# Optimization experiments

Hardware: AMD Instinct MI355X
Metric: run time of the kernel (lower is better)

The kernel has to match this reference:

```python
import jax, jax.numpy as jnp
import numpy as np

TOP_K = 2
NUM_EXPERTS = 8
ROUTE_SCALE = 1.0


def setup_inputs() -> dict:
    key = jax.random.key(0)
    ks = jax.random.split(key, 8)
    bs, slen, dim, hidden, E = 4, 1024, 2048, 1024, NUM_EXPERTS
    s = 0.02
    return {
        "x": jax.random.normal(ks[0], (bs, slen, dim), jnp.float32),
        "gate_w": jax.random.normal(ks[1], (E, dim), jnp.float32) * s,
        "w1": jax.random.normal(ks[2], (E, hidden, dim), jnp.float32) * s,
        "w2": jax.random.normal(ks[3], (E, dim, hidden), jnp.float32) * s,
        "w3": jax.random.normal(ks[4], (E, hidden, dim), jnp.float32) * s,
        "ws1": jax.random.normal(ks[5], (hidden, dim), jnp.float32) * s,
        "ws2": jax.random.normal(ks[6], (dim, hidden), jnp.float32) * s,
        "ws3": jax.random.normal(ks[7], (hidden, dim), jnp.float32) * s,
    }


def reference(x, gate_w, w1, w2, w3, ws1, ws2, ws3):
    bs, slen, dim = x.shape
    xf = x.reshape(-1, dim)  # (T, dim)
    # --- router: sigmoid scores in fp32, top-k (expert_bias is zeros at init) ---
    logits = (xf @ gate_w.T).astype(jnp.float32)  # (T, E)
    scores = jax.nn.sigmoid(logits)
    top_scores, sel_idx = jax.lax.top_k(scores, TOP_K)  # (T, k), (T, k)
    top_scores = top_scores * ROUTE_SCALE  # route_norm=False
    # --- routed experts: score_before_experts=True -> scale input by score ---
    routed = jnp.zeros_like(xf)
    for k in range(TOP_K):
        xs = xf * top_scores[:, k][:, None]  # (T, dim)
        h1 = jnp.einsum('td,ehd->teh', xs, w1)
        h3 = jnp.einsum('td,ehd->teh', xs, w3)
        h = jax.nn.silu(h1) * h3  # (T, E, hidden)
        onehot = jax.nn.one_hot(sel_idx[:, k], NUM_EXPERTS, dtype=h.dtype)  # (T, E)
        routed = routed + jnp.einsum('teh,te,edh->td', h, onehot, w2)
    # --- shared expert (SwiGLU FFN) ---
    shared = (jax.nn.silu(xf @ ws1.T) * (xf @ ws3.T)) @ ws2.T
    out = (shared + routed).reshape(bs, slen, dim)
    return out
```

## Files before the change

kernel.cpp:

```cpp
#include <hip/hip_runtime.h>
#include <hip/hip_bf16.h>
#include <cstdint>

#define TTOK   4096
#define DIM    2048
#define HID    1024
#define NEXP   8
#define GROWS  12288

typedef __attribute__((ext_vector_type(8))) __bf16 bf16x8;
typedef __attribute__((ext_vector_type(4))) float  f32x4;

__device__ __forceinline__ void glds16(const void* g, void* l) {
  __builtin_amdgcn_global_load_lds((const __attribute__((address_space(1))) void*)g,
                                   (__attribute__((address_space(3))) void*)l,
                                   16, 0, 0);
}

#define BAR() do { asm volatile("" ::: "memory"); __builtin_amdgcn_s_barrier(); \
                   asm volatile("" ::: "memory"); } while (0)

__global__ void convert_router_k(const float* __restrict__ w1, const float* __restrict__ w2,
                                 const float* __restrict__ w3, const float* __restrict__ ws1,
                                 const float* __restrict__ ws2, const float* __restrict__ ws3,
                                 __bf16* __restrict__ w13, __bf16* __restrict__ w2c,
                                 const float* __restrict__ x, const float* __restrict__ gw,
                                 int* __restrict__ sel, float* __restrict__ sco,
                                 int* __restrict__ counts) {
  const int N1 = 9 * 2048 * 2048 / 8;
  const int N2 = 9 * 2048 * 1024 / 8;
  const int CONV_BLOCKS = (N1 + N2) / 256;

  if (blockIdx.x < (unsigned)CONV_BLOCKS) {
    int s = blockIdx.x * 256 + threadIdx.x;
    const float* src;
    __bf16* dst;
    if (s < N1) {
      int e  = s / 524288;
      int r  = (s % 524288) / 256;
      int c  = (s % 256) * 8;
      int nr;
      if (r < 1024) { src = (e < 8 ? w1 + ((size_t)e * 1024 + r) * 2048 : ws1 + (size_t)r * 2048) + c;
                      nr = 2 * r; }
      else          { src = (e < 8 ? w3 + ((size_t)e * 1024 + (r - 1024)) * 2048 : ws3 + (size_t)(r - 1024) * 2048) + c;
                      nr = 2 * (r - 1024) + 1; }
      dst = w13 + ((size_t)e * 2048 + nr) * 2048 + c;
    } else {
      int s2 = s - N1;
      int e  = s2 / 262144;
      int r  = (s2 % 262144) / 128;
      int c  = (s2 % 128) * 8;
      src = (e < 8 ? w2 + ((size_t)e * 2048 + r) * 1024 : ws2 + (size_t)r * 1024) + c;
      dst = w2c + ((size_t)e * 2048 + r) * 1024 + c;
    }
    float4 a = *(const float4*)(src);
    float4 b = *(const float4*)(src + 4);
    bf16x8 o;
    o[0]=(__bf16)a.x; o[1]=(__bf16)a.y; o[2]=(__bf16)a.z; o[3]=(__bf16)a.w;
    o[4]=(__bf16)b.x; o[5]=(__bf16)b.y; o[6]=(__bf16)b.z; o[7]=(__bf16)b.w;
    *(bf16x8*)dst = o;
    return;
  }

  int t    = (blockIdx.x - CONV_BLOCKS) * 4 + (threadIdx.x >> 6);
  int lane = threadIdx.x & 63;
  const float* xr = x + (size_t)t * DIM;
  float acc[NEXP];
  #pragma unroll
  for (int e = 0; e < NEXP; ++e) acc[e] = 0.f;
  for (int d = lane * 4; d < DIM; d += 256) {
    float4 xv = *(const float4*)(xr + d);
    #pragma unroll
    for (int e = 0; e < NEXP; ++e) {
      float4 gv = *(const float4*)(gw + (size_t)e * DIM + d);
      acc[e] += xv.x * gv.x + xv.y * gv.y + xv.z * gv.z + xv.w * gv.w;
    }
  }
  #pragma unroll
  for (int off = 32; off; off >>= 1)
    #pragma unroll
    for (int e = 0; e < NEXP; ++e) acc[e] += __shfl_xor(acc[e], off);
  if (lane == 0) {
    float s[NEXP];
    #pragma unroll
    for (int e = 0; e < NEXP; ++e) s[e] = 1.f / (1.f + expf(-acc[e]));
    int e0 = 0;
    #pragma unroll
    for (int e = 1; e < NEXP; ++e) if (s[e] > s[e0]) e0 = e;
    int e1 = (e0 == 0) ? 1 : 0;
    #pragma unroll
    for (int e = 0; e < NEXP; ++e) if (e != e0 && s[e] > s[e1]) e1 = e;
    sel[2 * t] = e0; sel[2 * t + 1] = e1;
    sco[2 * t] = s[e0]; sco[2 * t + 1] = s[e1];
    atomicAdd(&counts[e0], 1); atomicAdd(&counts[e1], 1);
  }
}

__global__ void scan_k(const int* __restrict__ counts, int* __restrict__ offs) {
  if (threadIdx.x == 0 && blockIdx.x == 0) {
    int o = 0;
    for (int e = 0; e < NEXP; ++e) { offs[e] = o; o += counts[e]; }
    offs[NEXP] = o;
    offs[NEXP + 1] = o + TTOK;
  }
}

__global__ void gather_k(const float* __restrict__ x, const int* __restrict__ sel,
                         const float* __restrict__ sco, const int* __restrict__ offs,
                         int* __restrict__ cursor, int* __restrict__ token_rows,
                         __bf16* __restrict__ xg) {
  __shared__ int   rows[3];
  __shared__ float ss[3];
  int t = blockIdx.x;
  if (threadIdx.x == 0) {
    int e0 = sel[2 * t], e1 = sel[2 * t + 1];
    int r0 = offs[e0] + atomicAdd(&cursor[e0], 1);
    int r1 = offs[e1] + atomicAdd(&cursor[e1], 1);
    int r2 = 8192 + t;
    rows[0] = r0; rows[1] = r1; rows[2] = r2;
    ss[0] = sco[2 * t]; ss[1] = sco[2 * t + 1]; ss[2] = 1.0f;
    token_rows[3 * t] = r0; token_rows[3 * t + 1] = r1; token_rows[3 * t + 2] = r2;
  }
  __syncthreads();
  int c = threadIdx.x * 8;
  float4 v0 = *(const float4*)(x + (size_t)t * DIM + c);
  float4 v1 = *(const float4*)(x + (size_t)t * DIM + c + 4);
  #pragma unroll
  for (int j = 0; j < 3; ++j) {
    float s = ss[j];
    bf16x8 o;
    o[0]=(__bf16)(v0.x*s); o[1]=(__bf16)(v0.y*s); o[2]=(__bf16)(v0.z*s); o[3]=(__bf16)(v0.w*s);
    o[4]=(__bf16)(v1.x*s); o[5]=(__bf16)(v1.y*s); o[6]=(__bf16)(v1.z*s); o[7]=(__bf16)(v1.w*s);
    *(bf16x8*)(xg + (size_t)rows[j] * DIM + c) = o;
  }
}

template <int EPI>
__launch_bounds__(256)
__global__ void gemm_nt(const __bf16* __restrict__ A, const __bf16* __restrict__ Bw,
                        __bf16* __restrict__ Hb, float* __restrict__ c2a, float* __restrict__ c2b,
                        const int* __restrict__ offs, int K_, int N_) {
  int z  = blockIdx.z;
  int o0 = offs[z];
  int ne = offs[z + 1] - o0;

  int flat = blockIdx.y * 32 + blockIdx.x;
  int nid  = (flat & 7) * 64 + (flat >> 3);
  int bm   = nid & 31;
  int bn   = nid >> 5;

  if (bm * 128 >= ne) return;

  const __bf16* Aseg = A  + (size_t)(o0 + bm * 128) * K_;
  const __bf16* Bseg = Bw + ((size_t)z * N_ + bn * 128) * K_;

  __shared__ __align__(16) __bf16 sA[2][128 * 64];
  __shared__ __align__(16) __bf16 sB[2][128 * 64];

  int tid  = threadIdx.x;
  int wave = tid >> 6, lane = tid & 63;
  int wm = wave & 1, wn = wave >> 1;
  int fr = lane & 15;
  int fq = lane >> 4;
  int sw = fr & 7;

  f32x4 acc[4][4];
  #pragma unroll
  for (int i = 0; i < 4; ++i)
    #pragma unroll
    for (int j = 0; j < 4; ++j) acc[i][j] = (f32x4){0.f, 0.f, 0.f, 0.f};

#define STAGE(buf, kbase)                                                     \
  {                                                                           \
    _Pragma("unroll")                                                         \
    for (int it = 0; it < 4; ++it) {                                          \
      int s   = it * 256 + tid;                                               \
      int row = s >> 3;                                                       \
      int c8  = (s & 7) ^ (row & 7);                                          \
      glds16(Aseg + (size_t)row * K_ + (kbase) + c8 * 8, &sA[buf][s * 8]);    \
      glds16(Bseg + (size_t)row * K_ + (kbase) + c8 * 8, &sB[buf][s * 8]);    \
    }                                                                         \
  }

  STAGE(0, 0)
  asm volatile("s_waitcnt vmcnt(0)" ::: "memory");
  BAR();

  const int nk = K_ >> 6;
  for (int t = 0; t < nk; ++t) {
    int cur = t & 1;
    if (t + 1 < nk) {
      STAGE(cur ^ 1, (t + 1) << 6)
      asm volatile("s_waitcnt vmcnt(8)" ::: "memory");
    } else {
      asm volatile("s_waitcnt vmcnt(0)" ::: "memory");
    }
    BAR();

    const __bf16* rAbase = &sA[cur][(wm * 64 + fr) * 64];
    const __bf16* rBbase = &sB[cur][(wn * 64 + fr) * 64];
    #pragma unroll
    for (int kk = 0; kk < 2; ++kk) {
      int slot = ((kk * 4 + fq) ^ sw) * 8;
      bf16x8 af[4], bb[4];
      #pragma unroll
      for (int i = 0; i < 4; ++i) af[i] = *(const bf16x8*)(rAbase + i * 16 * 64 + slot);
      #pragma unroll
      for (int i = 0; i < 4; ++i) bb[i] = *(const bf16x8*)(rBbase + i * 16 * 64 + slot);
      #pragma unroll
      for (int mi = 0; mi < 4; ++mi)
        #pragma unroll
        for (int ni = 0; ni < 4; ++ni)
          acc[mi][ni] = __builtin_amdgcn_mfma_f32_16x16x32_bf16(af[mi], bb[ni], acc[mi][ni], 0, 0, 0);
    }
    BAR();
  }
#undef STAGE

  #pragma unroll
  for (int mi = 0; mi < 4; ++mi) {
    #pragma unroll
    for (int r = 0; r < 4; ++r) {
      int rl = bm * 128 + wm * 64 + mi * 16 + fq * 4 + r;
      bool ok = rl < ne;
      int grow = o0 + rl;
      if (EPI == 0) {
        #pragma unroll
        for (int ni = 0; ni < 4; ++ni) {
          float v = acc[mi][ni][r];
          float o = __shfl_xor(v, 1);
          float h1 = (fr & 1) ? o : v;
          float h3 = (fr & 1) ? v : o;
          float g  = h1 / (1.f + expf(-h1)) * h3;
          if (ok && !(fr & 1)) {
            int hcol = bn * 64 + wn * 32 + ni * 8 + (fr >> 1);
            Hb[(size_t)grow * 1024 + hcol] = (__bf16)g;
          }
        }
      } else {
        if (ok) {
          float* dst = (grow < 8192) ? (c2a + (size_t)grow * 2048)
                                     : (c2b + (size_t)(grow - 8192) * 2048);
          #pragma unroll
          for (int ni = 0; ni < 4; ++ni) {
            int col = bn * 128 + wn * 64 + ni * 16 + fr;
            dst[col] = acc[mi][ni][r];
          }
        }
      }
    }
  }
}

__global__ void combine_k(const float* __restrict__ c2a, const float* __restrict__ c2b,
                          const int* __restrict__ token_rows, float* __restrict__ out) {
  __shared__ int rr[3];
  int t = blockIdx.x;
  if (threadIdx.x < 3) rr[threadIdx.x] = token_rows[3 * t + threadIdx.x];
  __syncthreads();
  int c = threadIdx.x * 8;
  const float* p0 = c2a + (size_t)rr[0] * 2048 + c;
  const float* p1 = c2a + (size_t)rr[1] * 2048 + c;
  const float* p2 = c2b + (size_t)(rr[2] - 8192) * 2048 + c;
  float4 a0 = *(const float4*)p0,       a1 = *(const float4*)p1,       a2 = *(const float4*)p2;
  float4 b0 = *(const float4*)(p0 + 4), b1 = *(const float4*)(p1 + 4), b2 = *(const float4*)(p2 + 4);
  float4 oa, ob;
  oa.x = a0.x + a1.x + a2.x; oa.y = a0.y + a1.y + a2.y;
  oa.z = a0.z + a1.z + a2.z; oa.w = a0.w + a1.w + a2.w;
  ob.x = b0.x + b1.x + b2.x; ob.y = b0.y + b1.y + b2.y;
  ob.z = b0.z + b1.z + b2.z; ob.w = b0.w + b1.w + b2.w;
  float* op = out + (size_t)t * 2048 + c;
  *(float4*)op = oa;
  *(float4*)(op + 4) = ob;
}

extern "C" void kernel_launch(void* const* d_in, const int* in_sizes, int n_in,
                              void* d_out, int out_size, void* d_ws, size_t ws_size,
                              hipStream_t stream) {
  const float* x   = (const float*)d_in[0];
  const float* gw  = (const float*)d_in[1];
  const float* w1  = (const float*)d_in[2];
  const float* w2  = (const float*)d_in[3];
  const float* w3  = (const float*)d_in[4];
  const float* ws1 = (const float*)d_in[5];
  const float* ws2 = (const float*)d_in[6];
  const float* ws3 = (const float*)d_in[7];
  float* out = (float*)d_out;

  char* p = (char*)d_ws;
  int*   counts     = (int*)p;
  int*   cursor     = (int*)(p + 64);
  int*   offs       = (int*)(p + 128);
  int*   sel        = (int*)(p + 1024);
  float* sco        = (float*)(p + 1024 + 32768);
  int*   token_rows = (int*)(p + 1024 + 65536);
  char* big = p + (1 << 20);
  __bf16* w13  = (__bf16*)big;
  __bf16* w2c  = (__bf16*)(big + 75497472ull);
  __bf16* xg   = (__bf16*)(big + 75497472ull + 37748736ull);
  __bf16* hbuf = (__bf16*)(big + 75497472ull + 37748736ull + 50331648ull);
  float*  c2a  = (float*)w13;
  float*  c2b  = (float*)xg;

  hipMemsetAsync(p, 0, 256, stream);

  convert_router_k<<<27648 + TTOK / 4, 256, 0, stream>>>(w1, w2, w3, ws1, ws2, ws3, w13, w2c,
                                                         x, gw, sel, sco, counts);
  scan_k<<<1, 64, 0, stream>>>(counts, offs);
  gather_k<<<TTOK, 256, 0, stream>>>(x, sel, sco, offs, cursor, token_rows, xg);
  gemm_nt<0><<<dim3(32, 16, 9), 256, 0, stream>>>(xg, w13, hbuf, nullptr, nullptr, offs, 2048, 2048);
  gemm_nt<1><<<dim3(32, 16, 9), 256, 0, stream>>>(hbuf, w2c, nullptr, c2a, c2b, offs, 1024, 2048);
  combine_k<<<TTOK, 256, 0, stream>>>(c2a, c2b, token_rows, out);
}
```

Before: 743.4 us.

## Fuse combine into down-projection GEMM via atomic adds and unroll K loop

Drops the separate combine kernel and its fp32 intermediate buffers. The down-projection GEMM now scatters its results into the zeroed output through a row-to-token map, using scalar float atomicAdd. The double-buffered K loop is also manually unrolled by two with named shared buffers, which removes the dynamic buffer indexing. The cost is an extra memset of the output plus about 3x4096x2048 scalar atomics. This makes summation order nondeterministic and may add atomic contention or traffic.

```diff
diff --git a/kernel.cpp b/kernel.cpp
--- a/kernel.cpp
+++ b/kernel.cpp
@@ -107,7 +107,7 @@
 
 __global__ void gather_k(const float* __restrict__ x, const int* __restrict__ sel,
                          const float* __restrict__ sco, const int* __restrict__ offs,
-                         int* __restrict__ cursor, int* __restrict__ token_rows,
+                         int* __restrict__ cursor, int* __restrict__ row_token,
                          __bf16* __restrict__ xg) {
   __shared__ int   rows[3];
   __shared__ float ss[3];
@@ -119,7 +119,7 @@
     int r2 = 8192 + t;
     rows[0] = r0; rows[1] = r1; rows[2] = r2;
     ss[0] = sco[2 * t]; ss[1] = sco[2 * t + 1]; ss[2] = 1.0f;
-    token_rows[3 * t] = r0; token_rows[3 * t + 1] = r1; token_rows[3 * t + 2] = r2;
+    row_token[r0] = t; row_token[r1] = t; row_token[r2] = t;
   }
   __syncthreads();
   int c = threadIdx.x * 8;
@@ -138,7 +138,8 @@
 template <int EPI>
 __launch_bounds__(256)
 __global__ void gemm_nt(const __bf16* __restrict__ A, const __bf16* __restrict__ Bw,
-                        __bf16* __restrict__ Hb, float* __restrict__ c2a, float* __restrict__ c2b,
+                        __bf16* __restrict__ Hb, float* __restrict__ out,
+                        const int* __restrict__ row_token,
                         const int* __restrict__ offs, int K_, int N_) {
   int z  = blockIdx.z;
   int o0 = offs[z];
@@ -154,8 +155,10 @@
   const __bf16* Aseg = A  + (size_t)(o0 + bm * 128) * K_;
   const __bf16* Bseg = Bw + ((size_t)z * N_ + bn * 128) * K_;
 
-  __shared__ __align__(16) __bf16 sA[2][128 * 64];
-  __shared__ __align__(16) __bf16 sB[2][128 * 64];
+  __shared__ __align__(16) __bf16 sA0[128 * 64];
+  __shared__ __align__(16) __bf16 sB0[128 * 64];
+  __shared__ __align__(16) __bf16 sA1[128 * 64];
+  __shared__ __align__(16) __bf16 sB1[128 * 64];
 
   int tid  = threadIdx.x;
   int wave = tid >> 6, lane = tid & 63;
@@ -170,52 +173,67 @@
     #pragma unroll
     for (int j = 0; j < 4; ++j) acc[i][j] = (f32x4){0.f, 0.f, 0.f, 0.f};
 
-#define STAGE(buf, kbase)                                                     \
+#define STAGE(dA, dB, kbase)                                                  \
   {                                                                           \
     _Pragma("unroll")                                                         \
     for (int it = 0; it < 4; ++it) {                                          \
       int s   = it * 256 + tid;                                               \
       int row = s >> 3;                                                       \
       int c8  = (s & 7) ^ (row & 7);                                          \
-      glds16(Aseg + (size_t)row * K_ + (kbase) + c8 * 8, &sA[buf][s * 8]);    \
-      glds16(Bseg + (size_t)row * K_ + (kbase) + c8 * 8, &sB[buf][s * 8]);    \
+      glds16(Aseg + (size_t)row * K_ + (kbase) + c8 * 8, &dA[s * 8]);         \
+      glds16(Bseg + (size_t)row * K_ + (kbase) + c8 * 8, &dB[s * 8]);         \
     }                                                                         \
   }
 
-  STAGE(0, 0)
+#define COMPUTE(pA, pB)                                                       \
+  {                                                                           \
+    const __bf16* rAbase = pA + (wm * 64 + fr) * 64;                          \
+    const __bf16* rBbase = pB + (wn * 64 + fr) * 64;                          \
+    _Pragma("unroll")                                                         \
+    for (int kk = 0; kk < 2; ++kk) {                                          \
+      int slot = ((kk * 4 + fq) ^ sw) * 8;                                    \
+      bf16x8 af[4], bb[4];                                                    \
+      _Pragma("unroll")                                                       \
+      for (int i = 0; i < 4; ++i) af[i] = *(const bf16x8*)(rAbase + i * 16 * 64 + slot); \
+      _Pragma("unroll")                                                       \
+      for (int i = 0; i < 4; ++i) bb[i] = *(const bf16x8*)(rBbase + i * 16 * 64 + slot); \
+      _Pragma("unroll")                                                       \
+      for (int mi = 0; mi < 4; ++mi)                                          \
+        _Pragma("unroll")                                                     \
+        for (int ni = 0; ni < 4; ++ni)                                        \
+          acc[mi][ni] = __builtin_amdgcn_mfma_f32_16x16x32_bf16(af[mi], bb[ni], acc[mi][ni], 0, 0, 0); \
+    }                                                                         \
+  }
+
+  STAGE(sA0, sB0, 0)
   asm volatile("s_waitcnt vmcnt(0)" ::: "memory");
   BAR();
 
   const int nk = K_ >> 6;
-  for (int t = 0; t < nk; ++t) {
-    int cur = t & 1;
+  for (int t = 0; t < nk; t += 2) {
     if (t + 1 < nk) {
-      STAGE(cur ^ 1, (t + 1) << 6)
+      STAGE(sA1, sB1, (t + 1) << 6)
       asm volatile("s_waitcnt vmcnt(8)" ::: "memory");
     } else {
       asm volatile("s_waitcnt vmcnt(0)" ::: "memory");
     }
     BAR();
-
-    const __bf16* rAbase = &sA[cur][(wm * 64 + fr) * 64];
-    const __bf16* rBbase = &sB[cur][(wn * 64 + fr) * 64];
-    #pragma unroll
-    for (int kk = 0; kk < 2; ++kk) {
-      int slot = ((kk * 4 + fq) ^ sw) * 8;
-      bf16x8 af[4], bb[4];
-      #pragma unroll
-      for (int i = 0; i < 4; ++i) af[i] = *(const bf16x8*)(rAbase + i * 16 * 64 + slot);
-      #pragma unroll
-      for (int i = 0; i < 4; ++i) bb[i] = *(const bf16x8*)(rBbase + i * 16 * 64 + slot);
-      #pragma unroll
-      for (int mi = 0; mi < 4; ++mi)
-        #pragma unroll
-        for (int ni = 0; ni < 4; ++ni)
-          acc[mi][ni] = __builtin_amdgcn_mfma_f32_16x16x32_bf16(af[mi], bb[ni], acc[mi][ni], 0, 0, 0);
-    }
+    COMPUTE(sA0, sB0)
     BAR();
+    if (t + 1 < nk) {
+      if (t + 2 < nk) {
+        STAGE(sA0, sB0, (t + 2) << 6)
+        asm volatile("s_waitcnt vmcnt(8)" ::: "memory");
+      } else {
+        asm volatile("s_waitcnt vmcnt(0)" ::: "memory");
+      }
+      BAR();
+      COMPUTE(sA1, sB1)
+      BAR();
+    }
   }
 #undef STAGE
+#undef COMPUTE
 
   #pragma unroll
   for (int mi = 0; mi < 4; ++mi) {
@@ -239,39 +257,17 @@
         }
       } else {
         if (ok) {
-          float* dst = (grow < 8192) ? (c2a + (size_t)grow * 2048)
-                                     : (c2b + (size_t)(grow - 8192) * 2048);
+          int tok = row_token[grow];
+          float* dst = out + (size_t)tok * 2048;
           #pragma unroll
           for (int ni = 0; ni < 4; ++ni) {
             int col = bn * 128 + wn * 64 + ni * 16 + fr;
-            dst[col] = acc[mi][ni][r];
+            atomicAdd(&dst[col], acc[mi][ni][r]);
           }
         }
       }
     }
   }
-}
-
-__global__ void combine_k(const float* __restrict__ c2a, const float* __restrict__ c2b,
-                          const int* __restrict__ token_rows, float* __restrict__ out) {
-  __shared__ int rr[3];
-  int t = blockIdx.x;
-  if (threadIdx.x < 3) rr[threadIdx.x] = token_rows[3 * t + threadIdx.x];
-  __syncthreads();
-  int c = threadIdx.x * 8;
-  const float* p0 = c2a + (size_t)rr[0] * 2048 + c;
-  const float* p1 = c2a + (size_t)rr[1] * 2048 + c;
-  const float* p2 = c2b + (size_t)(rr[2] - 8192) * 2048 + c;
-  float4 a0 = *(const float4*)p0,       a1 = *(const float4*)p1,       a2 = *(const float4*)p2;
-  float4 b0 = *(const float4*)(p0 + 4), b1 = *(const float4*)(p1 + 4), b2 = *(const float4*)(p2 + 4);
-  float4 oa, ob;
-  oa.x = a0.x + a1.x + a2.x; oa.y = a0.y + a1.y + a2.y;
-  oa.z = a0.z + a1.z + a2.z; oa.w = a0.w + a1.w + a2.w;
-  ob.x = b0.x + b1.x + b2.x; ob.y = b0.y + b1.y + b2.y;
-  ob.z = b0.z + b1.z + b2.z; ob.w = b0.w + b1.w + b2.w;
-  float* op = out + (size_t)t * 2048 + c;
-  *(float4*)op = oa;
-  *(float4*)(op + 4) = ob;
 }
 
 extern "C" void kernel_launch(void* const* d_in, const int* in_sizes, int n_in,
@@ -288,27 +284,25 @@
   float* out = (float*)d_out;
 
   char* p = (char*)d_ws;
-  int*   counts     = (int*)p;
-  int*   cursor     = (int*)(p + 64);
-  int*   offs       = (int*)(p + 128);
-  int*   sel        = (int*)(p + 1024);
-  float* sco        = (float*)(p + 1024 + 32768);
-  int*   token_rows = (int*)(p + 1024 + 65536);
+  int*   counts    = (int*)p;
+  int*   cursor    = (int*)(p + 64);
+  int*   offs      = (int*)(p + 128);
+  int*   sel       = (int*)(p + 1024);
+  float* sco       = (float*)(p + 1024 + 32768);
+  int*   row_token = (int*)(p + 1024 + 65536);
   char* big = p + (1 << 20);
   __bf16* w13  = (__bf16*)big;
   __bf16* w2c  = (__bf16*)(big + 75497472ull);
   __bf16* xg   = (__bf16*)(big + 75497472ull + 37748736ull);
   __bf16* hbuf = (__bf16*)(big + 75497472ull + 37748736ull + 50331648ull);
-  float*  c2a  = (float*)w13;
-  float*  c2b  = (float*)xg;
 
   hipMemsetAsync(p, 0, 256, stream);
+  hipMemsetAsync(out, 0, (size_t)TTOK * DIM * sizeof(float), stream);
 
   convert_router_k<<<27648 + TTOK / 4, 256, 0, stream>>>(w1, w2, w3, ws1, ws2, ws3, w13, w2c,
                                                          x, gw, sel, sco, counts);
   scan_k<<<1, 64, 0, stream>>>(counts, offs);
-  gather_k<<<TTOK, 256, 0, stream>>>(x, sel, sco, offs, cursor, token_rows, xg);
+  gather_k<<<TTOK, 256, 0, stream>>>(x, sel, sco, offs, cursor, row_token, xg);
   gemm_nt<0><<<dim3(32, 16, 9), 256, 0, stream>>>(xg, w13, hbuf, nullptr, nullptr, offs, 2048, 2048);
-  gemm_nt<1><<<dim3(32, 16, 9), 256, 0, stream>>>(hbuf, w2c, nullptr, c2a, c2b, offs, 1024, 2048);
-  combine_k<<<TTOK, 256, 0, stream>>>(c2a, c2b, token_rows, out);
-}
+  gemm_nt<1><<<dim3(32, 16, 9), 256, 0, stream>>>(hbuf, w2c, nullptr, out, row_token, offs, 1024, 2048);
+}
```

New measurement: 762.6 us. +2.6%, slower.
